# Kernel tuning notes

Measured on AMD Instinct MI355X. Metric: run time of the kernel, lower is better.

Reference implementation:

```python
import jax, jax.numpy as jnp
import numpy as np

N, E, G = 20000, 320000, 64
IN, ED, H, F, FC, NC = 6, 2, 4, 64, 64, 2
HF = H * F


def _glorot(key, shape):
    fan_in, fan_out = shape[0], shape[-1]
    s = jnp.sqrt(6.0 / (fan_in + fan_out))
    return jax.random.uniform(key, shape, jnp.float32, -s, s)


def setup_inputs() -> dict:
    key = jax.random.key(0)
    ks = jax.random.split(key, 24)
    inp = {
        "x": jax.random.normal(ks[0], (N, IN), jnp.float32),
        "edge_index": jax.random.randint(ks[1], (2, E), 0, N, jnp.int64),
        "edge_attr": jax.random.normal(ks[2], (E, ED), jnp.float32),
        "batch": jnp.sort(jax.random.randint(ks[3], (N,), 0, G, jnp.int64)),
        # layer 0 (GATv2, in=6 -> 4 heads x 64)
        "Wl0": _glorot(ks[4], (IN, HF)), "bl0": jnp.zeros((HF,), jnp.float32),
        "Wr0": _glorot(ks[5], (IN, HF)), "br0": jnp.zeros((HF,), jnp.float32),
        "We0": _glorot(ks[6], (ED, HF)),
        "att0": _glorot(ks[7], (H, F)), "b0": jnp.zeros((HF,), jnp.float32),
        "proj0": _glorot(ks[8], (IN, HF)),  # residual projection 6 -> 256
        # layer 1 (GATv2, in=256 -> 4 heads x 64); residual is identity (256==256)
        "Wl1": _glorot(ks[9], (HF, HF)), "bl1": jnp.zeros((HF,), jnp.float32),
        "Wr1": _glorot(ks[10], (HF, HF)), "br1": jnp.zeros((HF,), jnp.float32),
        "We1": _glorot(ks[11], (ED, HF)),
        "att1": _glorot(ks[12], (H, F)), "b1": jnp.zeros((HF,), jnp.float32),
        # head
        "Wp": _glorot(ks[13], (HF, FC)), "bp": jnp.zeros((FC,), jnp.float32),
        "Wc": _glorot(ks[14], (FC, NC)), "bc": jnp.zeros((NC,), jnp.float32),
    }
    return inp


def _add_self_loops_mean(src, dst, eattr):
    # PyG add_self_loops(fill_value='mean'): self-loop attr = mean of incoming edge_attr
    s = jax.ops.segment_sum(eattr, dst, num_segments=N)
    c = jax.ops.segment_sum(jnp.ones((eattr.shape[0], 1), eattr.dtype), dst, num_segments=N)
    loop_attr = s / jnp.maximum(c, 1.0)
    idx = jnp.arange(N, dtype=src.dtype)
    return (jnp.concatenate([src, idx]), jnp.concatenate([dst, idx]),
            jnp.concatenate([eattr, loop_attr], axis=0))


def _gatv2(x, src, dst, ee, Wl, bl, Wr, br, att, bias):
    # ee: precomputed edge projection [E2, H, F]
    xl = (x @ Wl + bl).reshape(N, H, F)   # source transform
    xr = (x @ Wr + br).reshape(N, H, F)   # target transform
    m = jax.nn.leaky_relu(xl[src] + xr[dst] + ee, 0.2)   # [E2, H, F]
    logits = jnp.einsum('ehf,hf->eh', m, att)            # [E2, H]
    mx = jax.ops.segment_max(logits, dst, num_segments=N)
    ex = jnp.exp(logits - mx[dst])
    den = jax.ops.segment_sum(ex, dst, num_segments=N)
    alpha = ex / den[dst]                                 # scatter-softmax over dst
    out = jax.ops.segment_sum(xl[src] * alpha[:, :, None], dst, num_segments=N)
    return out.reshape(N, HF) + bias


def reference(x, edge_index, edge_attr, batch,
              Wl0, bl0, Wr0, br0, We0, att0, b0, proj0,
              Wl1, bl1, Wr1, br1, We1, att1, b1,
              Wp, bp, Wc, bc):
    src, dst, eattr = _add_self_loops_mean(edge_index[0], edge_index[1], edge_attr)
    # layer 0 (residual: projected input); dropout is a no-op in eval mode
    h = _gatv2(x, src, dst, (eattr @ We0).reshape(-1, H, F), Wl0, bl0, Wr0, br0, att0, b0)
    x1 = jax.nn.elu(h) + x @ proj0
    # layer 1 (residual: identity)
    h = _gatv2(x1, src, dst, (eattr @ We1).reshape(-1, H, F), Wl1, bl1, Wr1, br1, att1, b1)
    x2 = jax.nn.elu(h) + x1
    # pre-pool MLP + global mean pool over graphs + classifier
    z = jax.nn.elu(x2 @ Wp + bp)                           # [N, FC]
    gs = jax.ops.segment_sum(z, batch, num_segments=G)
    gc = jax.ops.segment_sum(jnp.ones((N, 1), z.dtype), batch, num_segments=G)
    pooled = gs / jnp.maximum(gc, 1.0)                     # [G, FC]
    return pooled @ Wc + bc                                # [G, NC]
```

## Files before the change

kernel.cpp:

```cpp
#include <hip/hip_runtime.h>
#include <math.h>

#define NN   20000
#define NE   320000
#define NG   64
#define INF_ 6
#define EDF  2
#define NH   4
#define FD   64
#define HF   256
#define FCD  64
#define NCD  2
#define CAP  64

#define ZB   ((NN + 255) / 256)
#define WCB  512
#define L0B  ((NN + 3) / 4)

#define ROWLIM ((NN - 1) * 512)

typedef short bf16x8 __attribute__((ext_vector_type(8)));
typedef float f32x4  __attribute__((ext_vector_type(4)));
typedef float f32x2  __attribute__((ext_vector_type(2)));

static __device__ __forceinline__ unsigned short f2bf(float f) {
  unsigned u = __float_as_uint(f);
  unsigned r = 0x7fffu + ((u >> 16) & 1u);
  return (unsigned short)((u + r) >> 16);
}
static __device__ __forceinline__ float4 bf2f4(uint2 p) {
  float4 v;
  v.x = __uint_as_float(p.x << 16);
  v.y = __uint_as_float(p.x & 0xffff0000u);
  v.z = __uint_as_float(p.y << 16);
  v.w = __uint_as_float(p.y & 0xffff0000u);
  return v;
}
static __device__ __forceinline__ f32x2 bflo2(unsigned u) {
  f32x2 v;
  v.x = __uint_as_float(u << 16);
  v.y = __uint_as_float(u & 0xffff0000u);
  return v;
}


__global__ __launch_bounds__(256) void k_init(
    int* __restrict__ cnt, float* __restrict__ gpool, int* __restrict__ gcnt,
    const float* __restrict__ Wl1, const float* __restrict__ Wr1,
    unsigned short* __restrict__ Wsw,
    const float* __restrict__ x,
    const float* __restrict__ Wl0, const float* __restrict__ bl0,
    const float* __restrict__ Wr0, const float* __restrict__ br0,
    unsigned short* __restrict__ xlb, unsigned short* __restrict__ xrb) {
  int b = blockIdx.x;
  int t = threadIdx.x;
  if (b < ZB) {
    int i = b * 256 + t;
    if (i < NN) cnt[i] = 0;
  } else if (b == ZB) {
    for (int i = t; i < NG * FCD; i += 256) gpool[i] = 0.f;
    if (t < NG) gcnt[t] = 0;
  } else if (b < ZB + 1 + WCB) {
    int id = (b - ZB - 1) * 256 + t;
    int j = id & 7, lane = (id >> 3) & 63, kk8 = (id >> 9) & 7, ntg = id >> 12;
    int n = ntg * 16 + (lane & 15);
    int k = kk8 * 32 + (lane >> 4) * 8 + j;
    float v = (n < 256) ? Wl1[k * 256 + n] : Wr1[k * 256 + (n - 256)];
    Wsw[id] = f2bf(v);
  } else {
    int w = t >> 6, lane = t & 63;
    int n = (b - ZB - 1 - WCB) * 4 + w;
    if (n >= NN) return;
    int cb = lane << 2;
    float4 al = *(const float4*)&bl0[cb];
    float4 ar = *(const float4*)&br0[cb];
#pragma unroll
    for (int k = 0; k < INF_; ++k) {
      float xv = x[n * INF_ + k];
      float4 wl = *(const float4*)&Wl0[k * HF + cb];
      float4 wr = *(const float4*)&Wr0[k * HF + cb];
      al.x = fmaf(xv, wl.x, al.x); al.y = fmaf(xv, wl.y, al.y);
      al.z = fmaf(xv, wl.z, al.z); al.w = fmaf(xv, wl.w, al.w);
      ar.x = fmaf(xv, wr.x, ar.x); ar.y = fmaf(xv, wr.y, ar.y);
      ar.z = fmaf(xv, wr.z, ar.z); ar.w = fmaf(xv, wr.w, ar.w);
    }
    uint2 pk;
    pk.x = (unsigned)f2bf(al.x) | ((unsigned)f2bf(al.y) << 16);
    pk.y = (unsigned)f2bf(al.z) | ((unsigned)f2bf(al.w) << 16);
    *(uint2*)&xlb[(size_t)n * HF + cb] = pk;
    uint2 pr;
    pr.x = (unsigned)f2bf(ar.x) | ((unsigned)f2bf(ar.y) << 16);
    pr.y = (unsigned)f2bf(ar.z) | ((unsigned)f2bf(ar.w) << 16);
    *(uint2*)&xrb[(size_t)n * HF + cb] = pr;
  }
}


__global__ void k_scatter(const int* __restrict__ ei, const float* __restrict__ ea,
                          int* __restrict__ cnt, uint2* __restrict__ rec) {
  int i = blockIdx.x * blockDim.x + threadIdx.x;
  if (i >= NE) return;
  int s = ei[i], d = ei[NE + i];
  float2 a = *(const float2*)&ea[2 * i];
  int pos = atomicAdd(&cnt[d], 1);
  if (pos < CAP)
    rec[(size_t)d * CAP + pos] = make_uint2((unsigned)(s * 512),
                                            (unsigned)f2bf(a.x) | ((unsigned)f2bf(a.y) << 16));
}


__global__ __launch_bounds__(256) void k_l1_mfma(
    const unsigned short* __restrict__ x1b,
    const unsigned short* __restrict__ Wsw,
    const float* __restrict__ bl, const float* __restrict__ br,
    unsigned short* __restrict__ xlb, unsigned short* __restrict__ xrb) {
  __shared__ unsigned short so[64][264];
  int t = threadIdx.x;
  int row0 = blockIdx.x * 64;
  int w = t >> 6, lane = t & 63;
  int quad = lane >> 4, ln = lane & 15;
  int y = blockIdx.y;
  const float* bias = y ? br : bl;
  unsigned short* dst = y ? xrb : xlb;

  int arow = row0 + w * 16 + ln; if (arow >= NN) arow = NN - 1;
  const unsigned short* aptr = x1b + (size_t)arow * HF + quad * 8;

  f32x4 acc[16];
#pragma unroll
  for (int i = 0; i < 16; ++i) acc[i] = (f32x4){0.f, 0.f, 0.f, 0.f};

  for (int kk8 = 0; kk8 < 8; ++kk8) {
    bf16x8 af = *(const bf16x8*)(aptr + kk8 * 32);
#pragma unroll
    for (int nt = 0; nt < 16; ++nt) {
      bf16x8 bfr = *(const bf16x8*)&Wsw[(size_t)((((y * 16 + nt) * 8 + kk8) * 64) + lane) * 8];
      acc[nt] = __builtin_amdgcn_mfma_f32_16x16x32_bf16(af, bfr, acc[nt], 0, 0, 0);
    }
  }
#pragma unroll
  for (int nt = 0; nt < 16; ++nt) {
    float bv = bias[nt * 16 + ln];
#pragma unroll
    for (int rg = 0; rg < 4; ++rg)
      so[w * 16 + quad * 4 + rg][nt * 16 + ln] = f2bf(acc[nt][rg] + bv);
  }
  __syncthreads();
#pragma unroll
  for (int i = 0; i < 8; ++i) {
    int idx = i * 256 + t;
    int row = idx >> 5, c8 = idx & 31;
    int grow = row0 + row;
    if (grow < NN)
      *(uint4*)&dst[(size_t)grow * HF + c8 * 8] = *(const uint4*)&so[row][c8 * 8];
  }
}


template <bool L0>
__global__ __launch_bounds__(256) void k_agg(
    const unsigned short* __restrict__ xlb, const unsigned short* xrb_,
    const int* __restrict__ cnt, const uint2* __restrict__ rec,
    const float* __restrict__ att, const float* __restrict__ We,
    const float* __restrict__ bias,
    const float* __restrict__ x, const float* __restrict__ proj0,
    unsigned short* __restrict__ x1bout,
    const unsigned short* __restrict__ x1bin, unsigned short* x2bout) {
  int wid = (blockIdx.x * 256 + threadIdx.x) >> 6;
  if (wid >= NN) return;
  int lane = threadIdx.x & 63;
  int n = wid;
  int cb = lane << 2;
  unsigned cbb = (unsigned)(cb << 1);

  const char* xlbase = (const char*)xlb;

  int nreal = min(cnt[n], CAP);
  int lastE = nreal - 1;
  const uint2* recn = rec + (size_t)n * CAP;

  float a0s = 0.f, a1s = 0.f;
  if (lane < nreal) {
    uint2 r = recn[lane];
    a0s = __uint_as_float(r.y << 16);
    a1s = __uint_as_float(r.y & 0xffff0000u);
  }
  uint2 ps = *(const uint2*)(xlbase + ((unsigned)(n * 512) + cbb));

  float4 xr4 = bf2f4(*(const uint2*)&xrb_[(size_t)n * HF + cb]);
  float4 at4 = *(const float4*)&att[cb];
  float4 w04 = *(const float4*)&We[cb];
  float4 w14 = *(const float4*)&We[HF + cb];
  f32x2 xrA = {xr4.x, xr4.y}, xrB = {xr4.z, xr4.w};
  f32x2 atA = {at4.x, at4.y}, atB = {at4.z, at4.w};
  f32x2 w0A = {w04.x, w04.y}, w0B = {w04.z, w04.w};
  f32x2 w1A = {w14.x, w14.y}, w1B = {w14.z, w14.w};

  f32x2 accA = {0.f, 0.f}, accB = {0.f, 0.f};
  float den = 0.f;

  for (int e0 = 0; e0 < nreal; e0 += 4) {
    uint4 q0 = *(const uint4*)&recn[e0];
    uint4 q1 = *(const uint4*)&recn[e0 + 2];
    unsigned off[4] = {q0.x, q0.z, q1.x, q1.z};
    unsigned atr[4] = {q0.y, q0.w, q1.y, q1.w};
    uint2 p4[4];
#pragma unroll
    for (int i = 0; i < 4; ++i) {
      unsigned o = min(off[i], (unsigned)ROWLIM) & 0xfffffe00u;
      p4[i] = *(const uint2*)(xlbase + (o + cbb));
    }

    float t4[4];
#pragma unroll
    for (int i = 0; i < 4; ++i) {
      float a0 = __uint_as_float(atr[i] << 16);
      float a1 = __uint_as_float(atr[i] & 0xffff0000u);
      f32x2 a0v = {a0, a0}, a1v = {a1, a1};
      f32x2 mA = a1v * w1A + xrA; mA = a0v * w0A + mA;
      f32x2 mB = a1v * w1B + xrB; mB = a0v * w0B + mB;
      mA = mA + bflo2(p4[i].x);
      mB = mB + bflo2(p4[i].y);
      mA.x = fmaxf(mA.x, 0.2f * mA.x);
      mA.y = fmaxf(mA.y, 0.2f * mA.y);
      mB.x = fmaxf(mB.x, 0.2f * mB.x);
      mB.y = fmaxf(mB.y, 0.2f * mB.y);
      f32x2 d = mA * atA;
      d = mB * atB + d;
      t4[i] = d.x + d.y;
    }
#pragma unroll
    for (int o = 1; o <= 8; o <<= 1) {
#pragma unroll
      for (int i = 0; i < 4; ++i) t4[i] += __shfl_xor(t4[i], o, 64);
    }
#pragma unroll
    for (int i = 0; i < 4; ++i) {
      float w = (e0 + i <= lastE) ? __expf(fminf(t4[i], 80.f)) : 0.f;
      den += w;
      f32x2 wv = {w, w};
      accA = wv * bflo2(p4[i].x) + accA;
      accB = wv * bflo2(p4[i].y) + accB;
    }
  }

#pragma unroll
  for (int o = 32; o; o >>= 1) {
    a0s += __shfl_xor(a0s, o, 64);
    a1s += __shfl_xor(a1s, o, 64);
  }
  float im = 1.0f / fmaxf((float)nreal, 1.0f);
  float a0m = a0s * im, a1m = a1s * im;

  f32x2 vSA = bflo2(ps.x), vSB = bflo2(ps.y);
  {
    f32x2 a0v = {a0m, a0m}, a1v = {a1m, a1m};
    f32x2 mA = a1v * w1A + xrA; mA = a0v * w0A + mA;
    f32x2 mB = a1v * w1B + xrB; mB = a0v * w0B + mB;
    mA = mA + vSA; mB = mB + vSB;
    mA.x = fmaxf(mA.x, 0.2f * mA.x);
    mA.y = fmaxf(mA.y, 0.2f * mA.y);
    mB.x = fmaxf(mB.x, 0.2f * mB.x);
    mB.y = fmaxf(mB.y, 0.2f * mB.y);
    f32x2 d = mA * atA;
    d = mB * atB + d;
    float tS = d.x + d.y;
    tS += __shfl_xor(tS, 1, 64);
    tS += __shfl_xor(tS, 2, 64);
    tS += __shfl_xor(tS, 4, 64);
    tS += __shfl_xor(tS, 8, 64);
    float wS = __expf(fminf(tS, 80.f));
    den += wS;
    f32x2 wv = {wS, wS};
    accA = wv * vSA + accA;
    accB = wv * vSB + accB;
  }

  float inv = 1.0f / den;
  float4 b4 = *(const float4*)&bias[cb];
  float4 o;
  o.x = fmaf(accA.x, inv, b4.x);
  o.y = fmaf(accA.y, inv, b4.y);
  o.z = fmaf(accB.x, inv, b4.z);
  o.w = fmaf(accB.y, inv, b4.w);
  o.x = (o.x > 0.f) ? o.x : expm1f(o.x);
  o.y = (o.y > 0.f) ? o.y : expm1f(o.y);
  o.z = (o.z > 0.f) ? o.z : expm1f(o.z);
  o.w = (o.w > 0.f) ? o.w : expm1f(o.w);

  if (L0) {
    f32x2 rA = {0.f, 0.f}, rB = {0.f, 0.f};
#pragma unroll
    for (int k = 0; k < INF_; ++k) {
      float xv = x[n * INF_ + k];
      float4 p = *(const float4*)&proj0[k * HF + cb];
      f32x2 xvv = {xv, xv};
      f32x2 pA = {p.x, p.y}, pB = {p.z, p.w};
      rA = xvv * pA + rA;
      rB = xvv * pB + rB;
    }
    o.x += rA.x; o.y += rA.y; o.z += rB.x; o.w += rB.y;
    uint2 pk;
    pk.x = (unsigned)f2bf(o.x) | ((unsigned)f2bf(o.y) << 16);
    pk.y = (unsigned)f2bf(o.z) | ((unsigned)f2bf(o.w) << 16);
    *(uint2*)&x1bout[(size_t)n * HF + cb] = pk;
  } else {
    float4 x1v = bf2f4(*(const uint2*)&x1bin[(size_t)n * HF + cb]);
    o.x += x1v.x; o.y += x1v.y; o.z += x1v.z; o.w += x1v.w;
    uint2 pk;
    pk.x = (unsigned)f2bf(o.x) | ((unsigned)f2bf(o.y) << 16);
    pk.y = (unsigned)f2bf(o.z) | ((unsigned)f2bf(o.w) << 16);
    *(uint2*)&x2bout[(size_t)n * HF + cb] = pk;
  }
}


__global__ __launch_bounds__(256) void k_pool(
    const unsigned short* __restrict__ x2b, const float* __restrict__ Wp,
    const float* __restrict__ bp, const int* __restrict__ batch,
    float* __restrict__ gpool, int* __restrict__ gcnt) {
  __shared__ float xs[32 * HF];
  __shared__ int gid_s[32];
  int t = threadIdx.x;
  int row0 = blockIdx.x * 32;
  const uint4* s4 = (const uint4*)(x2b + (size_t)row0 * HF);
#pragma unroll
  for (int i = 0; i < 4; ++i) {
    int idx = i * 256 + t;
    uint4 p = s4[idx];
    int base = idx * 8;
    float4 lo = bf2f4(make_uint2(p.x, p.y));
    float4 hi = bf2f4(make_uint2(p.z, p.w));
    *(float4*)&xs[base] = lo;
    *(float4*)&xs[base + 4] = hi;
  }
  if (t < 32) gid_s[t] = batch[row0 + t];
  __syncthreads();
  int j = t & 63, rg = t >> 6;
  float acc[8];
#pragma unroll
  for (int rr = 0; rr < 8; ++rr) acc[rr] = 0.f;
  for (int k4 = 0; k4 < HF / 4; ++k4) {
    float w0 = Wp[(k4 * 4 + 0) * FCD + j];
    float w1 = Wp[(k4 * 4 + 1) * FCD + j];
    float w2 = Wp[(k4 * 4 + 2) * FCD + j];
    float w3 = Wp[(k4 * 4 + 3) * FCD + j];
#pragma unroll
    for (int rr = 0; rr < 8; ++rr) {
      float4 xv = *(const float4*)&xs[(rg * 8 + rr) * HF + k4 * 4];
      acc[rr] = fmaf(xv.x, w0, acc[rr]);
      acc[rr] = fmaf(xv.y, w1, acc[rr]);
      acc[rr] = fmaf(xv.z, w2, acc[rr]);
      acc[rr] = fmaf(xv.w, w3, acc[rr]);
    }
  }
  float b = bp[j];
  int gprev = gid_s[rg * 8];
  float run = 0.f;
  int rcnt = 0;
#pragma unroll
  for (int rr = 0; rr < 8; ++rr) {
    float a = acc[rr] + b;
    float z = (a > 0.f) ? a : expm1f(a);
    int g = gid_s[rg * 8 + rr];
    if (g != gprev) {
      atomicAdd(&gpool[gprev * FCD + j], run);
      if (j == 0) atomicAdd(&gcnt[gprev], rcnt);
      run = 0.f; rcnt = 0; gprev = g;
    }
    run += z; ++rcnt;
  }
  atomicAdd(&gpool[gprev * FCD + j], run);
  if (j == 0) atomicAdd(&gcnt[gprev], rcnt);
}


__global__ void k_head(const float* __restrict__ gpool, const int* __restrict__ gcnt,
                       const float* __restrict__ Wc, const float* __restrict__ bc,
                       float* __restrict__ out) {
  int t = threadIdx.x;
  int g = t >> 1, k = t & 1;
  float inv = 1.0f / fmaxf((float)gcnt[g], 1.0f);
  float a = bc[k];
#pragma unroll
  for (int j = 0; j < FCD; ++j)
    a = fmaf(gpool[g * FCD + j] * inv, Wc[j * NCD + k], a);
  out[g * NCD + k] = a;
}


extern "C" void kernel_launch(void* const* d_in, const int* in_sizes, int n_in,
                              void* d_out, int out_size, void* d_ws, size_t ws_size,
                              hipStream_t stream) {
  const float* x    = (const float*)d_in[0];
  const int*   ei   = (const int*)d_in[1];
  const float* ea   = (const float*)d_in[2];
  const int*   batch= (const int*)d_in[3];
  const float* Wl0  = (const float*)d_in[4];
  const float* bl0  = (const float*)d_in[5];
  const float* Wr0  = (const float*)d_in[6];
  const float* br0  = (const float*)d_in[7];
  const float* We0  = (const float*)d_in[8];
  const float* att0 = (const float*)d_in[9];
  const float* b0   = (const float*)d_in[10];
  const float* proj0= (const float*)d_in[11];
  const float* Wl1  = (const float*)d_in[12];
  const float* bl1  = (const float*)d_in[13];
  const float* Wr1  = (const float*)d_in[14];
  const float* br1  = (const float*)d_in[15];
  const float* We1  = (const float*)d_in[16];
  const float* att1 = (const float*)d_in[17];
  const float* b1   = (const float*)d_in[18];
  const float* Wp   = (const float*)d_in[19];
  const float* bp   = (const float*)d_in[20];
  const float* Wc   = (const float*)d_in[21];
  const float* bc   = (const float*)d_in[22];
  float* out = (float*)d_out;

  char* ws = (char*)d_ws;
  size_t off = 0;
  int*   cnt    = (int*)(ws + off);   off += (NN * 4 + 15) / 16 * 16;
  uint2* rec    = (uint2*)(ws + off); off += (size_t)NN * CAP * 8;
  unsigned short* xlb = (unsigned short*)(ws + off); off += (size_t)NN * HF * 2;
  unsigned short* xrb = (unsigned short*)(ws + off); off += (size_t)NN * HF * 2;
  unsigned short* x1b = (unsigned short*)(ws + off); off += (size_t)NN * HF * 2;
  float* gpool  = (float*)(ws + off); off += NG * FCD * 4;
  unsigned short* Wsw = (unsigned short*)(ws + off); off += 512 * 256 * 2;
  int*   gcnt   = (int*)(ws + off);   off += (NG * 4 + 15) / 16 * 16;
  unsigned short* x2b = xrb;
  (void)ws_size; (void)in_sizes; (void)n_in; (void)out_size;

  k_init<<<ZB + 1 + WCB + L0B, 256, 0, stream>>>(
      cnt, gpool, gcnt, Wl1, Wr1, Wsw, x, Wl0, bl0, Wr0, br0, xlb, xrb);

  k_scatter<<<(NE + 255) / 256, 256, 0, stream>>>(ei, ea, cnt, rec);

  k_agg<true><<<(NN * 64 + 255) / 256, 256, 0, stream>>>(
      xlb, xrb, cnt, rec, att0, We0, b0, x, proj0, x1b, nullptr, nullptr);

  k_l1_mfma<<<dim3((NN + 63) / 64, 2), 256, 0, stream>>>(x1b, Wsw, bl1, br1, xlb, xrb);
  k_agg<false><<<(NN * 64 + 255) / 256, 256, 0, stream>>>(
      xlb, xrb, cnt, rec, att1, We1, b1, nullptr, nullptr, nullptr, x1b, x2b);

  k_pool<<<NN / 32, 256, 0, stream>>>(x2b, Wp, bp, batch, gpool, gcnt);
  k_head<<<1, 128, 0, stream>>>(gpool, gcnt, Wc, bc, out);
}
```

Before: 270.4 us.

## Convert kernels to persistent grid-stride loops with fixed block counts

Every kernel (init, scatter, both aggregation passes, the MFMA GEMM, pooling) now launches a fixed number of blocks and loops over its work with a grid-stride loop, where before it launched one block per work item. In the aggregation kernel the per-wave constants (att, We, bias) are hoisted out of the node loop. Leaky ReLU is applied with a vector max helper. The aim is to cut block launch and scheduling overhead and to reuse the hoisted loads. In exchange, load balance may get worse: the fixed grid sizes may not fill the GPU evenly, and the MFMA kernel now has a serial tile loop with 256 blocks.

```diff
diff --git a/kernel.cpp b/kernel.cpp
--- a/kernel.cpp
+++ b/kernel.cpp
@@ -13,11 +13,19 @@
 #define NCD  2
 #define CAP  64
 
-#define ZB   ((NN + 255) / 256)
-#define WCB  512
-#define L0B  ((NN + 3) / 4)
-
 #define ROWLIM ((NN - 1) * 512)
+
+#define AGG_BLK  2048
+#define AGG_WAVES (AGG_BLK * 4)
+#define SCAT_BLK 512
+#define POOL_BLK 256
+#define MFMA_BLK 256
+#define NTILES   ((NN + 63) / 64)
+
+#define CZB      80
+#define WCB2     128
+#define L0BLK    1072
+#define INIT_BLK (CZB + WCB2 + L0BLK)
 
 typedef short bf16x8 __attribute__((ext_vector_type(8)));
 typedef float f32x4  __attribute__((ext_vector_type(4)));
@@ -41,6 +49,9 @@
   v.x = __uint_as_float(u << 16);
   v.y = __uint_as_float(u & 0xffff0000u);
   return v;
+}
+static __device__ __forceinline__ f32x2 lky(f32x2 v) {
+  return __builtin_elementwise_max(v, v * 0.2f);
 }
 
 
@@ -54,58 +65,61 @@
     unsigned short* __restrict__ xlb, unsigned short* __restrict__ xrb) {
   int b = blockIdx.x;
   int t = threadIdx.x;
-  if (b < ZB) {
+  if (b < CZB) {
     int i = b * 256 + t;
     if (i < NN) cnt[i] = 0;
-  } else if (b == ZB) {
-    for (int i = t; i < NG * FCD; i += 256) gpool[i] = 0.f;
-    if (t < NG) gcnt[t] = 0;
-  } else if (b < ZB + 1 + WCB) {
-    int id = (b - ZB - 1) * 256 + t;
-    int j = id & 7, lane = (id >> 3) & 63, kk8 = (id >> 9) & 7, ntg = id >> 12;
-    int n = ntg * 16 + (lane & 15);
-    int k = kk8 * 32 + (lane >> 4) * 8 + j;
-    float v = (n < 256) ? Wl1[k * 256 + n] : Wr1[k * 256 + (n - 256)];
-    Wsw[id] = f2bf(v);
+    if (b == 0) {
+      for (int i2 = t; i2 < NG * FCD; i2 += 256) gpool[i2] = 0.f;
+      if (t < NG) gcnt[t] = 0;
+    }
+  } else if (b < CZB + WCB2) {
+    for (int id = (b - CZB) * 256 + t; id < 512 * 256; id += WCB2 * 256) {
+      int j = id & 7, lane = (id >> 3) & 63, kk8 = (id >> 9) & 7, ntg = id >> 12;
+      int n = ntg * 16 + (lane & 15);
+      int k = kk8 * 32 + (lane >> 4) * 8 + j;
+      float v = (n < 256) ? Wl1[k * 256 + n] : Wr1[k * 256 + (n - 256)];
+      Wsw[id] = f2bf(v);
+    }
   } else {
     int w = t >> 6, lane = t & 63;
-    int n = (b - ZB - 1 - WCB) * 4 + w;
-    if (n >= NN) return;
     int cb = lane << 2;
-    float4 al = *(const float4*)&bl0[cb];
-    float4 ar = *(const float4*)&br0[cb];
-#pragma unroll
-    for (int k = 0; k < INF_; ++k) {
-      float xv = x[n * INF_ + k];
-      float4 wl = *(const float4*)&Wl0[k * HF + cb];
-      float4 wr = *(const float4*)&Wr0[k * HF + cb];
-      al.x = fmaf(xv, wl.x, al.x); al.y = fmaf(xv, wl.y, al.y);
-      al.z = fmaf(xv, wl.z, al.z); al.w = fmaf(xv, wl.w, al.w);
-      ar.x = fmaf(xv, wr.x, ar.x); ar.y = fmaf(xv, wr.y, ar.y);
-      ar.z = fmaf(xv, wr.z, ar.z); ar.w = fmaf(xv, wr.w, ar.w);
-    }
-    uint2 pk;
-    pk.x = (unsigned)f2bf(al.x) | ((unsigned)f2bf(al.y) << 16);
-    pk.y = (unsigned)f2bf(al.z) | ((unsigned)f2bf(al.w) << 16);
-    *(uint2*)&xlb[(size_t)n * HF + cb] = pk;
-    uint2 pr;
-    pr.x = (unsigned)f2bf(ar.x) | ((unsigned)f2bf(ar.y) << 16);
-    pr.y = (unsigned)f2bf(ar.z) | ((unsigned)f2bf(ar.w) << 16);
-    *(uint2*)&xrb[(size_t)n * HF + cb] = pr;
+    for (int n = (b - CZB - WCB2) * 4 + w; n < NN; n += L0BLK * 4) {
+      float4 al = *(const float4*)&bl0[cb];
+      float4 ar = *(const float4*)&br0[cb];
+#pragma unroll
+      for (int k = 0; k < INF_; ++k) {
+        float xv = x[n * INF_ + k];
+        float4 wl = *(const float4*)&Wl0[k * HF + cb];
+        float4 wr = *(const float4*)&Wr0[k * HF + cb];
+        al.x = fmaf(xv, wl.x, al.x); al.y = fmaf(xv, wl.y, al.y);
+        al.z = fmaf(xv, wl.z, al.z); al.w = fmaf(xv, wl.w, al.w);
+        ar.x = fmaf(xv, wr.x, ar.x); ar.y = fmaf(xv, wr.y, ar.y);
+        ar.z = fmaf(xv, wr.z, ar.z); ar.w = fmaf(xv, wr.w, ar.w);
+      }
+      uint2 pk;
+      pk.x = (unsigned)f2bf(al.x) | ((unsigned)f2bf(al.y) << 16);
+      pk.y = (unsigned)f2bf(al.z) | ((unsigned)f2bf(al.w) << 16);
+      *(uint2*)&xlb[(size_t)n * HF + cb] = pk;
+      uint2 pr;
+      pr.x = (unsigned)f2bf(ar.x) | ((unsigned)f2bf(ar.y) << 16);
+      pr.y = (unsigned)f2bf(ar.z) | ((unsigned)f2bf(ar.w) << 16);
+      *(uint2*)&xrb[(size_t)n * HF + cb] = pr;
+    }
   }
 }
 
 
-__global__ void k_scatter(const int* __restrict__ ei, const float* __restrict__ ea,
-                          int* __restrict__ cnt, uint2* __restrict__ rec) {
-  int i = blockIdx.x * blockDim.x + threadIdx.x;
-  if (i >= NE) return;
-  int s = ei[i], d = ei[NE + i];
-  float2 a = *(const float2*)&ea[2 * i];
-  int pos = atomicAdd(&cnt[d], 1);
-  if (pos < CAP)
-    rec[(size_t)d * CAP + pos] = make_uint2((unsigned)(s * 512),
-                                            (unsigned)f2bf(a.x) | ((unsigned)f2bf(a.y) << 16));
+__global__ __launch_bounds__(256) void k_scatter(
+    const int* __restrict__ ei, const float* __restrict__ ea,
+    int* __restrict__ cnt, uint2* __restrict__ rec) {
+  for (int i = blockIdx.x * 256 + threadIdx.x; i < NE; i += SCAT_BLK * 256) {
+    int s = ei[i], d = ei[NE + i];
+    float2 a = *(const float2*)&ea[2 * i];
+    int pos = atomicAdd(&cnt[d], 1);
+    if (pos < CAP)
+      rec[(size_t)d * CAP + pos] = make_uint2((unsigned)(s * 512),
+                                              (unsigned)f2bf(a.x) | ((unsigned)f2bf(a.y) << 16));
+  }
 }
 
 
@@ -116,43 +130,47 @@
     unsigned short* __restrict__ xlb, unsigned short* __restrict__ xrb) {
   __shared__ unsigned short so[64][264];
   int t = threadIdx.x;
-  int row0 = blockIdx.x * 64;
   int w = t >> 6, lane = t & 63;
   int quad = lane >> 4, ln = lane & 15;
-  int y = blockIdx.y;
-  const float* bias = y ? br : bl;
-  unsigned short* dst = y ? xrb : xlb;
-
-  int arow = row0 + w * 16 + ln; if (arow >= NN) arow = NN - 1;
-  const unsigned short* aptr = x1b + (size_t)arow * HF + quad * 8;
-
-  f32x4 acc[16];
-#pragma unroll
-  for (int i = 0; i < 16; ++i) acc[i] = (f32x4){0.f, 0.f, 0.f, 0.f};
-
-  for (int kk8 = 0; kk8 < 8; ++kk8) {
-    bf16x8 af = *(const bf16x8*)(aptr + kk8 * 32);
+
+  for (int v = blockIdx.x; v < NTILES * 2; v += MFMA_BLK) {
+    int row0 = (v >> 1) * 64;
+    int y = v & 1;
+    const float* bias = y ? br : bl;
+    unsigned short* dst = y ? xrb : xlb;
+
+    int arow = row0 + w * 16 + ln; if (arow >= NN) arow = NN - 1;
+    const unsigned short* aptr = x1b + (size_t)arow * HF + quad * 8;
+
+    f32x4 acc[16];
+#pragma unroll
+    for (int i = 0; i < 16; ++i) acc[i] = (f32x4){0.f, 0.f, 0.f, 0.f};
+
+    for (int kk8 = 0; kk8 < 8; ++kk8) {
+      bf16x8 af = *(const bf16x8*)(aptr + kk8 * 32);
+#pragma unroll
+      for (int nt = 0; nt < 16; ++nt) {
+        bf16x8 bfr = *(const bf16x8*)&Wsw[(size_t)((((y * 16 + nt) * 8 + kk8) * 64) + lane) * 8];
+        acc[nt] = __builtin_amdgcn_mfma_f32_16x16x32_bf16(af, bfr, acc[nt], 0, 0, 0);
+      }
+    }
 #pragma unroll
     for (int nt = 0; nt < 16; ++nt) {
-      bf16x8 bfr = *(const bf16x8*)&Wsw[(size_t)((((y * 16 + nt) * 8 + kk8) * 64) + lane) * 8];
-      acc[nt] = __builtin_amdgcn_mfma_f32_16x16x32_bf16(af, bfr, acc[nt], 0, 0, 0);
-    }
-  }
-#pragma unroll
-  for (int nt = 0; nt < 16; ++nt) {
-    float bv = bias[nt * 16 + ln];
-#pragma unroll
-    for (int rg = 0; rg < 4; ++rg)
-      so[w * 16 + quad * 4 + rg][nt * 16 + ln] = f2bf(acc[nt][rg] + bv);
-  }
-  __syncthreads();
-#pragma unroll
-  for (int i = 0; i < 8; ++i) {
-    int idx = i * 256 + t;
-    int row = idx >> 5, c8 = idx & 31;
-    int grow = row0 + row;
-    if (grow < NN)
-      *(uint4*)&dst[(size_t)grow * HF + c8 * 8] = *(const uint4*)&so[row][c8 * 8];
+      float bv = bias[nt * 16 + ln];
+#pragma unroll
+      for (int rg = 0; rg < 4; ++rg)
+        so[w * 16 + quad * 4 + rg][nt * 16 + ln] = f2bf(acc[nt][rg] + bv);
+    }
+    __syncthreads();
+#pragma unroll
+    for (int i = 0; i < 8; ++i) {
+      int idx = i * 256 + t;
+      int row = idx >> 5, c8 = idx & 31;
+      int grow = row0 + row;
+      if (grow < NN)
+        *(uint4*)&dst[(size_t)grow * HF + c8 * 8] = *(const uint4*)&so[row][c8 * 8];
+    }
+    __syncthreads();
   }
 }
 
@@ -166,151 +184,144 @@
     const float* __restrict__ x, const float* __restrict__ proj0,
     unsigned short* __restrict__ x1bout,
     const unsigned short* __restrict__ x1bin, unsigned short* x2bout) {
-  int wid = (blockIdx.x * 256 + threadIdx.x) >> 6;
-  if (wid >= NN) return;
+  int wslot = (blockIdx.x << 2) + (threadIdx.x >> 6);
   int lane = threadIdx.x & 63;
-  int n = wid;
   int cb = lane << 2;
   unsigned cbb = (unsigned)(cb << 1);
-
   const char* xlbase = (const char*)xlb;
 
-  int nreal = min(cnt[n], CAP);
-  int lastE = nreal - 1;
-  const uint2* recn = rec + (size_t)n * CAP;
-
-  float a0s = 0.f, a1s = 0.f;
-  if (lane < nreal) {
-    uint2 r = recn[lane];
-    a0s = __uint_as_float(r.y << 16);
-    a1s = __uint_as_float(r.y & 0xffff0000u);
-  }
-  uint2 ps = *(const uint2*)(xlbase + ((unsigned)(n * 512) + cbb));
-
-  float4 xr4 = bf2f4(*(const uint2*)&xrb_[(size_t)n * HF + cb]);
   float4 at4 = *(const float4*)&att[cb];
   float4 w04 = *(const float4*)&We[cb];
   float4 w14 = *(const float4*)&We[HF + cb];
-  f32x2 xrA = {xr4.x, xr4.y}, xrB = {xr4.z, xr4.w};
+  float4 b4  = *(const float4*)&bias[cb];
   f32x2 atA = {at4.x, at4.y}, atB = {at4.z, at4.w};
   f32x2 w0A = {w04.x, w04.y}, w0B = {w04.z, w04.w};
   f32x2 w1A = {w14.x, w14.y}, w1B = {w14.z, w14.w};
 
-  f32x2 accA = {0.f, 0.f}, accB = {0.f, 0.f};
-  float den = 0.f;
-
-  for (int e0 = 0; e0 < nreal; e0 += 4) {
-    uint4 q0 = *(const uint4*)&recn[e0];
-    uint4 q1 = *(const uint4*)&recn[e0 + 2];
-    unsigned off[4] = {q0.x, q0.z, q1.x, q1.z};
-    unsigned atr[4] = {q0.y, q0.w, q1.y, q1.w};
-    uint2 p4[4];
-#pragma unroll
-    for (int i = 0; i < 4; ++i) {
-      unsigned o = min(off[i], (unsigned)ROWLIM) & 0xfffffe00u;
-      p4[i] = *(const uint2*)(xlbase + (o + cbb));
-    }
-
-    float t4[4];
-#pragma unroll
-    for (int i = 0; i < 4; ++i) {
-      float a0 = __uint_as_float(atr[i] << 16);
-      float a1 = __uint_as_float(atr[i] & 0xffff0000u);
-      f32x2 a0v = {a0, a0}, a1v = {a1, a1};
+  for (int n = wslot; n < NN; n += AGG_WAVES) {
+    int nreal = min(cnt[n], CAP);
+    int lastE = nreal - 1;
+    const uint2* recn = rec + (size_t)n * CAP;
+
+    float a0s = 0.f, a1s = 0.f;
+    if (lane < nreal) {
+      uint2 r = recn[lane];
+      a0s = __uint_as_float(r.y << 16);
+      a1s = __uint_as_float(r.y & 0xffff0000u);
+    }
+    uint2 ps = *(const uint2*)(xlbase + ((unsigned)(n * 512) + cbb));
+
+    float4 xr4 = bf2f4(*(const uint2*)&xrb_[(size_t)n * HF + cb]);
+    f32x2 xrA = {xr4.x, xr4.y}, xrB = {xr4.z, xr4.w};
+
+    f32x2 accA = {0.f, 0.f}, accB = {0.f, 0.f};
+    float den = 0.f;
+
+    for (int e0 = 0; e0 < nreal; e0 += 4) {
+      uint4 q0 = *(const uint4*)&recn[e0];
+      uint4 q1 = *(const uint4*)&recn[e0 + 2];
+      unsigned off[4] = {q0.x, q0.z, q1.x, q1.z};
+      unsigned atr[4] = {q0.y, q0.w, q1.y, q1.w};
+      uint2 p4[4];
+#pragma unroll
+      for (int i = 0; i < 4; ++i) {
+        unsigned o = min(off[i], (unsigned)ROWLIM) & 0xfffffe00u;
+        p4[i] = *(const uint2*)(xlbase + (o + cbb));
+      }
+
+      float t4[4];
+#pragma unroll
+      for (int i = 0; i < 4; ++i) {
+        float a0 = __uint_as_float(atr[i] << 16);
+        float a1 = __uint_as_float(atr[i] & 0xffff0000u);
+        f32x2 a0v = {a0, a0}, a1v = {a1, a1};
+        f32x2 mA = a1v * w1A + xrA; mA = a0v * w0A + mA;
+        f32x2 mB = a1v * w1B + xrB; mB = a0v * w0B + mB;
+        mA = lky(mA + bflo2(p4[i].x));
+        mB = lky(mB + bflo2(p4[i].y));
+        f32x2 d = mA * atA;
+        d = mB * atB + d;
+        t4[i] = d.x + d.y;
+      }
+#pragma unroll
+      for (int o = 1; o <= 8; o <<= 1) {
+#pragma unroll
+        for (int i = 0; i < 4; ++i) t4[i] += __shfl_xor(t4[i], o, 64);
+      }
+#pragma unroll
+      for (int i = 0; i < 4; ++i) {
+        float w = (e0 + i <= lastE) ? __expf(fminf(t4[i], 80.f)) : 0.f;
+        den += w;
+        f32x2 wv = {w, w};
+        accA = wv * bflo2(p4[i].x) + accA;
+        accB = wv * bflo2(p4[i].y) + accB;
+      }
+    }
+
+#pragma unroll
+    for (int o = 32; o; o >>= 1) {
+      a0s += __shfl_xor(a0s, o, 64);
+      a1s += __shfl_xor(a1s, o, 64);
+    }
+    float im = 1.0f / fmaxf((float)nreal, 1.0f);
+    float a0m = a0s * im, a1m = a1s * im;
+
+    f32x2 vSA = bflo2(ps.x), vSB = bflo2(ps.y);
+    {
+      f32x2 a0v = {a0m, a0m}, a1v = {a1m, a1m};
       f32x2 mA = a1v * w1A + xrA; mA = a0v * w0A + mA;
       f32x2 mB = a1v * w1B + xrB; mB = a0v * w0B + mB;
-      mA = mA + bflo2(p4[i].x);
-      mB = mB + bflo2(p4[i].y);
-      mA.x = fmaxf(mA.x, 0.2f * mA.x);
-      mA.y = fmaxf(mA.y, 0.2f * mA.y);
-      mB.x = fmaxf(mB.x, 0.2f * mB.x);
-      mB.y = fmaxf(mB.y, 0.2f * mB.y);
+      mA = lky(mA + vSA);
+      mB = lky(mB + vSB);
       f32x2 d = mA * atA;
       d = mB * atB + d;
-      t4[i] = d.x + d.y;
-    }
-#pragma unroll
-    for (int o = 1; o <= 8; o <<= 1) {
-#pragma unroll
-      for (int i = 0; i < 4; ++i) t4[i] += __shfl_xor(t4[i], o, 64);
-    }
-#pragma unroll
-    for (int i = 0; i < 4; ++i) {
-      float w = (e0 + i <= lastE) ? __expf(fminf(t4[i], 80.f)) : 0.f;
-      den += w;
-      f32x2 wv = {w, w};
-      accA = wv * bflo2(p4[i].x) + accA;
-      accB = wv * bflo2(p4[i].y) + accB;
-    }
-  }
-
-#pragma unroll
-  for (int o = 32; o; o >>= 1) {
-    a0s += __shfl_xor(a0s, o, 64);
-    a1s += __shfl_xor(a1s, o, 64);
-  }
-  float im = 1.0f / fmaxf((float)nreal, 1.0f);
-  float a0m = a0s * im, a1m = a1s * im;
-
-  f32x2 vSA = bflo2(ps.x), vSB = bflo2(ps.y);
-  {
-    f32x2 a0v = {a0m, a0m}, a1v = {a1m, a1m};
-    f32x2 mA = a1v * w1A + xrA; mA = a0v * w0A + mA;
-    f32x2 mB = a1v * w1B + xrB; mB = a0v * w0B + mB;
-    mA = mA + vSA; mB = mB + vSB;
-    mA.x = fmaxf(mA.x, 0.2f * mA.x);
-    mA.y = fmaxf(mA.y, 0.2f * mA.y);
-    mB.x = fmaxf(mB.x, 0.2f * mB.x);
-    mB.y = fmaxf(mB.y, 0.2f * mB.y);
-    f32x2 d = mA * atA;
-    d = mB * atB + d;
-    float tS = d.x + d.y;
-    tS += __shfl_xor(tS, 1, 64);
-    tS += __shfl_xor(tS, 2, 64);
-    tS += __shfl_xor(tS, 4, 64);
-    tS += __shfl_xor(tS, 8, 64);
-    float wS = __expf(fminf(tS, 80.f));
-    den += wS;
-    f32x2 wv = {wS, wS};
-    accA = wv * vSA + accA;
-    accB = wv * vSB + accB;
-  }
-
-  float inv = 1.0f / den;
-  float4 b4 = *(const float4*)&bias[cb];
-  float4 o;
-  o.x = fmaf(accA.x, inv, b4.x);
-  o.y = fmaf(accA.y, inv, b4.y);
-  o.z = fmaf(accB.x, inv, b4.z);
-  o.w = fmaf(accB.y, inv, b4.w);
-  o.x = (o.x > 0.f) ? o.x : expm1f(o.x);
-  o.y = (o.y > 0.f) ? o.y : expm1f(o.y);
-  o.z = (o.z > 0.f) ? o.z : expm1f(o.z);
-  o.w = (o.w > 0.f) ? o.w : expm1f(o.w);
-
-  if (L0) {
-    f32x2 rA = {0.f, 0.f}, rB = {0.f, 0.f};
-#pragma unroll
-    for (int k = 0; k < INF_; ++k) {
-      float xv = x[n * INF_ + k];
-      float4 p = *(const float4*)&proj0[k * HF + cb];
-      f32x2 xvv = {xv, xv};
-      f32x2 pA = {p.x, p.y}, pB = {p.z, p.w};
-      rA = xvv * pA + rA;
-      rB = xvv * pB + rB;
-    }
-    o.x += rA.x; o.y += rA.y; o.z += rB.x; o.w += rB.y;
-    uint2 pk;
-    pk.x = (unsigned)f2bf(o.x) | ((unsigned)f2bf(o.y) << 16);
-    pk.y = (unsigned)f2bf(o.z) | ((unsigned)f2bf(o.w) << 16);
-    *(uint2*)&x1bout[(size_t)n * HF + cb] = pk;
-  } else {
-    float4 x1v = bf2f4(*(const uint2*)&x1bin[(size_t)n * HF + cb]);
-    o.x += x1v.x; o.y += x1v.y; o.z += x1v.z; o.w += x1v.w;
-    uint2 pk;
-    pk.x = (unsigned)f2bf(o.x) | ((unsigned)f2bf(o.y) << 16);
-    pk.y = (unsigned)f2bf(o.z) | ((unsigned)f2bf(o.w) << 16);
-    *(uint2*)&x2bout[(size_t)n * HF + cb] = pk;
+      float tS = d.x + d.y;
+      tS += __shfl_xor(tS, 1, 64);
+      tS += __shfl_xor(tS, 2, 64);
+      tS += __shfl_xor(tS, 4, 64);
+      tS += __shfl_xor(tS, 8, 64);
+      float wS = __expf(fminf(tS, 80.f));
+      den += wS;
+      f32x2 wv = {wS, wS};
+      accA = wv * vSA + accA;
+      accB = wv * vSB + accB;
+    }
+
+    float inv = 1.0f / den;
+    float4 o;
+    o.x = fmaf(accA.x, inv, b4.x);
+    o.y = fmaf(accA.y, inv, b4.y);
+    o.z = fmaf(accB.x, inv, b4.z);
+    o.w = fmaf(accB.y, inv, b4.w);
+    o.x = (o.x > 0.f) ? o.x : expm1f(o.x);
+    o.y = (o.y > 0.f) ? o.y : expm1f(o.y);
+    o.z = (o.z > 0.f) ? o.z : expm1f(o.z);
+    o.w = (o.w > 0.f) ? o.w : expm1f(o.w);
+
+    if (L0) {
+      f32x2 rA = {0.f, 0.f}, rB = {0.f, 0.f};
+#pragma unroll
+      for (int k = 0; k < INF_; ++k) {
+        float xv = x[n * INF_ + k];
+        float4 p = *(const float4*)&proj0[k * HF + cb];
+        f32x2 xvv = {xv, xv};
+        f32x2 pA = {p.x, p.y}, pB = {p.z, p.w};
+        rA = xvv * pA + rA;
+        rB = xvv * pB + rB;
+      }
+      o.x += rA.x; o.y += rA.y; o.z += rB.x; o.w += rB.y;
+      uint2 pk;
+      pk.x = (unsigned)f2bf(o.x) | ((unsigned)f2bf(o.y) << 16);
+      pk.y = (unsigned)f2bf(o.z) | ((unsigned)f2bf(o.w) << 16);
+      *(uint2*)&x1bout[(size_t)n * HF + cb] = pk;
+    } else {
+      float4 x1v = bf2f4(*(const uint2*)&x1bin[(size_t)n * HF + cb]);
+      o.x += x1v.x; o.y += x1v.y; o.z += x1v.z; o.w += x1v.w;
+      uint2 pk;
+      pk.x = (unsigned)f2bf(o.x) | ((unsigned)f2bf(o.y) << 16);
+      pk.y = (unsigned)f2bf(o.z) | ((unsigned)f2bf(o.w) << 16);
+      *(uint2*)&x2bout[(size_t)n * HF + cb] = pk;
+    }
   }
 }
 
@@ -322,56 +333,59 @@
   __shared__ float xs[32 * HF];
   __shared__ int gid_s[32];
   int t = threadIdx.x;
-  int row0 = blockIdx.x * 32;
-  const uint4* s4 = (const uint4*)(x2b + (size_t)row0 * HF);
-#pragma unroll
-  for (int i = 0; i < 4; ++i) {
-    int idx = i * 256 + t;
-    uint4 p = s4[idx];
-    int base = idx * 8;
-    float4 lo = bf2f4(make_uint2(p.x, p.y));
-    float4 hi = bf2f4(make_uint2(p.z, p.w));
-    *(float4*)&xs[base] = lo;
-    *(float4*)&xs[base + 4] = hi;
+  int j = t & 63, rg = t >> 6;
+
+  for (int row0 = blockIdx.x * 32; row0 < NN; row0 += POOL_BLK * 32) {
+    const uint4* s4 = (const uint4*)(x2b + (size_t)row0 * HF);
+#pragma unroll
+    for (int i = 0; i < 4; ++i) {
+      int idx = i * 256 + t;
+      uint4 p = s4[idx];
+      int base = idx * 8;
+      float4 lo = bf2f4(make_uint2(p.x, p.y));
+      float4 hi = bf2f4(make_uint2(p.z, p.w));
+      *(float4*)&xs[base] = lo;
+      *(float4*)&xs[base + 4] = hi;
+    }
+    if (t < 32) gid_s[t] = batch[row0 + t];
+    __syncthreads();
+    float acc[8];
+#pragma unroll
+    for (int rr = 0; rr < 8; ++rr) acc[rr] = 0.f;
+    for (int k4 = 0; k4 < HF / 4; ++k4) {
+      float w0 = Wp[(k4 * 4 + 0) * FCD + j];
+      float w1 = Wp[(k4 * 4 + 1) * FCD + j];
+      float w2 = Wp[(k4 * 4 + 2) * FCD + j];
+      float w3 = Wp[(k4 * 4 + 3) * FCD + j];
+#pragma unroll
+      for (int rr = 0; rr < 8; ++rr) {
+        float4 xv = *(const float4*)&xs[(rg * 8 + rr) * HF + k4 * 4];
+        acc[rr] = fmaf(xv.x, w0, acc[rr]);
+        acc[rr] = fmaf(xv.y, w1, acc[rr]);
+        acc[rr] = fmaf(xv.z, w2, acc[rr]);
+        acc[rr] = fmaf(xv.w, w3, acc[rr]);
+      }
+    }
+    float b = bp[j];
+    int gprev = gid_s[rg * 8];
+    float run = 0.f;
+    int rcnt = 0;
+#pragma unroll
+    for (int rr = 0; rr < 8; ++rr) {
+      float a = acc[rr] + b;
+      float z = (a > 0.f) ? a : expm1f(a);
+      int g = gid_s[rg * 8 + rr];
+      if (g != gprev) {
+        atomicAdd(&gpool[gprev * FCD + j], run);
+        if (j == 0) atomicAdd(&gcnt[gprev], rcnt);
+        run = 0.f; rcnt = 0; gprev = g;
+      }
+      run += z; ++rcnt;
+    }
+    atomicAdd(&gpool[gprev * FCD + j], run);
+    if (j == 0) atomicAdd(&gcnt[gprev], rcnt);
+    __syncthreads();
   }
-  if (t < 32) gid_s[t] = batch[row0 + t];
-  __syncthreads();
-  int j = t & 63, rg = t >> 6;
-  float acc[8];
-#pragma unroll
-  for (int rr = 0; rr < 8; ++rr) acc[rr] = 0.f;
-  for (int k4 = 0; k4 < HF / 4; ++k4) {
-    float w0 = Wp[(k4 * 4 + 0) * FCD + j];
-    float w1 = Wp[(k4 * 4 + 1) * FCD + j];
-    float w2 = Wp[(k4 * 4 + 2) * FCD + j];
-    float w3 = Wp[(k4 * 4 + 3) * FCD + j];
-#pragma unroll
-    for (int rr = 0; rr < 8; ++rr) {
-      float4 xv = *(const float4*)&xs[(rg * 8 + rr) * HF + k4 * 4];
-      acc[rr] = fmaf(xv.x, w0, acc[rr]);
-      acc[rr] = fmaf(xv.y, w1, acc[rr]);
-      acc[rr] = fmaf(xv.z, w2, acc[rr]);
-      acc[rr] = fmaf(xv.w, w3, acc[rr]);
-    }
-  }
-  float b = bp[j];
-  int gprev = gid_s[rg * 8];
-  float run = 0.f;
-  int rcnt = 0;
-#pragma unroll
-  for (int rr = 0; rr < 8; ++rr) {
-    float a = acc[rr] + b;
-    float z = (a > 0.f) ? a : expm1f(a);
-    int g = gid_s[rg * 8 + rr];
-    if (g != gprev) {
-      atomicAdd(&gpool[gprev * FCD + j], run);
-      if (j == 0) atomicAdd(&gcnt[gprev], rcnt);
-      run = 0.f; rcnt = 0; gprev = g;
-    }
-    run += z; ++rcnt;
-  }
-  atomicAdd(&gpool[gprev * FCD + j], run);
-  if (j == 0) atomicAdd(&gcnt[gprev], rcnt);
 }
 
 
@@ -430,18 +444,18 @@
   unsigned short* x2b = xrb;
   (void)ws_size; (void)in_sizes; (void)n_in; (void)out_size;
 
-  k_init<<<ZB + 1 + WCB + L0B, 256, 0, stream>>>(
+  k_init<<<INIT_BLK, 256, 0, stream>>>(
       cnt, gpool, gcnt, Wl1, Wr1, Wsw, x, Wl0, bl0, Wr0, br0, xlb, xrb);
 
-  k_scatter<<<(NE + 255) / 256, 256, 0, stream>>>(ei, ea, cnt, rec);
-
-  k_agg<true><<<(NN * 64 + 255) / 256, 256, 0, stream>>>(
+  k_scatter<<<SCAT_BLK, 256, 0, stream>>>(ei, ea, cnt, rec);
+
+  k_agg<true><<<AGG_BLK, 256, 0, stream>>>(
       xlb, xrb, cnt, rec, att0, We0, b0, x, proj0, x1b, nullptr, nullptr);
 
-  k_l1_mfma<<<dim3((NN + 63) / 64, 2), 256, 0, stream>>>(x1b, Wsw, bl1, br1, xlb, xrb);
-  k_agg<false><<<(NN * 64 + 255) / 256, 256, 0, stream>>>(
+  k_l1_mfma<<<MFMA_BLK, 256, 0, stream>>>(x1b, Wsw, bl1, br1, xlb, xrb);
+  k_agg<false><<<AGG_BLK, 256, 0, stream>>>(
       xlb, xrb, cnt, rec, att1, We1, b1, nullptr, nullptr, nullptr, x1b, x2b);
 
-  k_pool<<<NN / 32, 256, 0, stream>>>(x2b, Wp, bp, batch, gpool, gcnt);
+  k_pool<<<POOL_BLK, 256, 0, stream>>>(x2b, Wp, bp, batch, gpool, gcnt);
   k_head<<<1, 128, 0, stream>>>(gpool, gcnt, Wc, bc, out);
 }
```

Result: slower. 330.4 us (+22.2%).
